# Performance work log

Hardware: AMD Instinct MI355X
Metric: run time of the kernel (lower is better)

The kernel has to match this reference:

```python
import jax, jax.numpy as jnp
import numpy as np

# MSDeformAttn dims inferred from Linear shapes: 8 heads * 4 levels * 2 points
H, L, P, D, C = 8, 4, 2, 32, 256
SHAPES = [(128, 128), (64, 64), (32, 32), (16, 16)]  # (H_l, W_l) per level
NV = sum(h * w for h, w in SHAPES)  # 21760
STARTS = np.cumsum([0] + [h * w for h, w in SHAPES])


def _bilinear(val, lx, ly, Hl, Wl):
    """grid_sample(align_corners=False, padding='zeros') equivalent.
    val: [B, H, Hl*Wl, D]; lx, ly: [B, H, N] normalized sample coords in [0,1].
    Returns [B, H, N, D]."""
    x = lx * Wl - 0.5
    y = ly * Hl - 0.5
    x0 = jnp.floor(x)
    y0 = jnp.floor(y)
    fx = x - x0
    fy = y - y0
    x0i = x0.astype(jnp.int32)
    y0i = y0.astype(jnp.int32)
    out = jnp.zeros(val.shape[:2] + (x.shape[-1], val.shape[-1]), val.dtype)
    corners = ((0, 0, (1 - fx) * (1 - fy)), (1, 0, fx * (1 - fy)),
               (0, 1, (1 - fx) * fy), (1, 1, fx * fy))
    for dx, dy, w in corners:
        xi = x0i + dx
        yi = y0i + dy
        valid = ((xi >= 0) & (xi < Wl) & (yi >= 0) & (yi < Hl)).astype(val.dtype)
        idx = jnp.clip(yi, 0, Hl - 1) * Wl + jnp.clip(xi, 0, Wl - 1)
        g = jnp.take_along_axis(val, idx[..., None], axis=2)  # [B,H,N,D]
        out = out + g * (w * valid)[..., None]
    return out


def setup_inputs() -> dict:
    key = jax.random.key(0)
    ks = jax.random.split(key, 8)
    B, NQ = 4, 1000
    s = 0.02
    return {
        "query": jax.random.normal(ks[0], (B, NQ, C), jnp.float32),
        "value": jax.random.normal(ks[1], (B, NV, C), jnp.float32),
        "reference_points": jax.random.uniform(ks[2], (B, NQ, L, 2), jnp.float32),
        "W_off": jax.random.normal(ks[3], (C, H * L * P * 2), jnp.float32) * s,
        "b_off": jnp.zeros((H * L * P * 2,), jnp.float32),
        "W_attn": jax.random.normal(ks[4], (C, H * L * P), jnp.float32) * s,
        "b_attn": jnp.zeros((H * L * P,), jnp.float32),
        "W_val": jax.random.normal(ks[5], (C, C), jnp.float32) * s,
        "b_val": jnp.zeros((C,), jnp.float32),
        "W_out": jax.random.normal(ks[6], (C, C), jnp.float32) * s,
        "b_out": jnp.zeros((C,), jnp.float32),
    }


def reference(query, value, reference_points, W_off, b_off, W_attn, b_attn,
              W_val, b_val, W_out, b_out):
    B, NQ, _ = query.shape
    # value projection -> per-head values [B, H, NV, D]
    v = (value @ W_val + b_val).reshape(B, NV, H, D).transpose(0, 2, 1, 3)
    # sampling offsets [B, NQ, H, L, P, 2]
    off = (query @ W_off + b_off).reshape(B, NQ, H, L, P, 2)
    # attention weights: softmax over L*P
    attn = jax.nn.softmax((query @ W_attn + b_attn).reshape(B, NQ, H, L * P), axis=-1)
    attn = attn.reshape(B, NQ, H, L, P)
    # normalizer (W_l, H_l) per level, matching Deformable-DETR
    wh = jnp.asarray([[w, h] for h, w in SHAPES], dtype=query.dtype)  # [L,2]
    loc = reference_points[:, :, None, :, None, :] + off / wh[None, None, None, :, None, :]
    out = jnp.zeros((B, H, NQ, D), dtype=query.dtype)
    for l, (hl, wl) in enumerate(SHAPES):
        vl = v[:, :, STARTS[l]:STARTS[l + 1], :]                 # [B,H,hl*wl,D]
        lx = loc[:, :, :, l, :, 0].transpose(0, 2, 1, 3).reshape(B, H, NQ * P)
        ly = loc[:, :, :, l, :, 1].transpose(0, 2, 1, 3).reshape(B, H, NQ * P)
        s = _bilinear(vl, lx, ly, hl, wl).reshape(B, H, NQ, P, D)
        al = attn[:, :, :, l, :].transpose(0, 2, 1, 3)           # [B,H,NQ,P]
        out = out + jnp.sum(s * al[..., None], axis=3)
    out = out.transpose(0, 2, 1, 3).reshape(B, NQ, C)
    return out @ W_out + b_out  # dropout(p=0) is identity
```

## Files before the change

### kernel.cpp

```cpp
#include <hip/hip_runtime.h>

#define HH 8
#define LL 4
#define PP 2
#define DD 32
#define CC 256
#define NVV 21760
#define NQQ 1000
#define BB 4
#define NQT (BB * NQQ)
#define NLOGB (NQT / 32)
#define NVALB ((BB * NVV) / 64)

typedef __attribute__((ext_vector_type(8))) short short8;
typedef __attribute__((ext_vector_type(4))) short shortv4;
typedef __attribute__((ext_vector_type(4))) float f32x4;

__device__ __forceinline__ unsigned short f2bf(float f) {
    unsigned u = __float_as_uint(f);
    u += 0x7FFF + ((u >> 16) & 1);
    return (unsigned short)(u >> 16);
}
__device__ __forceinline__ float bf2f(unsigned short h) {
    return __uint_as_float(((unsigned)h) << 16);
}
__device__ __forceinline__ unsigned cvtpk(float lo, float hi) {
    unsigned r;
    asm volatile("v_cvt_pk_bf16_f32 %0, %1, %2" : "=v"(r) : "v"(lo), "v"(hi));
    return r;
}

__device__ __forceinline__ void gload_lds16(const void* g, void* l) {
    __builtin_amdgcn_global_load_lds(
        (const __attribute__((address_space(1))) unsigned int*)g,
        (__attribute__((address_space(3))) unsigned int*)l, 16, 0, 0);
}

__global__ __launch_bounds__(256) void prep_kernel(
    const float* __restrict__ Wv, const float* __restrict__ Woff,
    const float* __restrict__ Wattn, const float* __restrict__ Wout,
    unsigned short* __restrict__ WTs, unsigned short* __restrict__ W1T,
    unsigned short* __restrict__ WoT)
{
    const int c = blockIdx.x;
    const int n = threadIdx.x;
    {
        int s = c >> 5, t = c & 31;
        WTs[s * 8192 + n * 32 + (t ^ (((n >> 1) & 3) << 3))] =
            f2bf(Wv[c * CC + n]);
    }
    if (n < 192) {
        float x = (n < 128) ? Woff[c * 128 + n] : Wattn[c * 64 + (n - 128)];
        W1T[n * CC + c] = f2bf(x);
    }
    WoT[n * CC + c] = f2bf(Wout[c * CC + n]);
}

__global__ __launch_bounds__(256, 3) void val_logits_fused(
    const float* __restrict__ value, const unsigned short* __restrict__ WTs,
    const float* __restrict__ bv, unsigned short* __restrict__ v_out,
    const float* __restrict__ query, const unsigned short* __restrict__ W1T,
    const float* __restrict__ b_off, const float* __restrict__ b_attn,
    float* __restrict__ logits)
{
    __shared__ __align__(16) char lds[49152];

    const int tid = threadIdx.x;
    const int lane = tid & 63;

    if (blockIdx.x >= NLOGB) {
        char (*Abuf)[8192] = (char (*)[8192])(lds);
        char (*Bbuf)[16384] = (char (*)[16384])(lds + 16384);

        const int w = tid >> 6;
        const int wm = w >> 1;
        const int wn = w & 1;
        const int lr = lane & 15;
        const int q = lane >> 4;
        const int bm = (blockIdx.x - NLOGB) * 64;

#define STAGE(s, bi)                                                        \
    {                                                                       \
        _Pragma("unroll") for (int r = 0; r < 2; ++r) {                     \
            int u = r * 256 + tid;                                          \
            int m = u >> 3, c = u & 7;                                      \
            gload_lds16((const char*)value + (size_t)(bm + m) * 1024 +      \
                            (s) * 128 + ((c ^ (m & 7)) * 16),               \
                        &Abuf[bi][u * 16]);                                 \
        }                                                                   \
        _Pragma("unroll") for (int r = 0; r < 4; ++r) {                     \
            int off = (r * 256 + tid) * 16;                                 \
            gload_lds16((const char*)WTs + (s) * 16384 + off,               \
                        &Bbuf[bi][off]);                                    \
        }                                                                   \
    }

        f32x4 acc[2][8] = {};

        STAGE(0, 0);
        STAGE(1, 1);

#pragma unroll
        for (int s = 0; s < 8; ++s) {
            const int cur = s & 1;
            if (s < 7) {
                asm volatile("s_waitcnt vmcnt(6)" ::: "memory");
            } else {
                asm volatile("s_waitcnt vmcnt(0)" ::: "memory");
            }
            __builtin_amdgcn_s_barrier();
            __builtin_amdgcn_sched_barrier(0);

            short8 af[2];
#pragma unroll
            for (int mf = 0; mf < 2; ++mf) {
                int m = wm * 32 + mf * 16 + lr;
                const char* base = &Abuf[cur][m * 128];
                f32x4 lo = *(const f32x4*)(base + (((2 * q) ^ (m & 7)) * 16));
                f32x4 hi =
                    *(const f32x4*)(base + (((2 * q + 1) ^ (m & 7)) * 16));
                uint4 uv = {cvtpk(lo[0], lo[1]), cvtpk(lo[2], lo[3]),
                            cvtpk(hi[0], hi[1]), cvtpk(hi[2], hi[3])};
                af[mf] = __builtin_bit_cast(short8, uv);
            }
#pragma unroll
            for (int nf = 0; nf < 8; ++nf) {
                int n = wn * 128 + nf * 16 + lr;
                short8 bf = *(const short8*)&Bbuf[cur]
                                [n * 64 + ((q ^ ((n >> 1) & 3)) * 16)];
                acc[0][nf] = __builtin_amdgcn_mfma_f32_16x16x32_bf16(
                    af[0], bf, acc[0][nf], 0, 0, 0);
                acc[1][nf] = __builtin_amdgcn_mfma_f32_16x16x32_bf16(
                    af[1], bf, acc[1][nf], 0, 0, 0);
            }

            __builtin_amdgcn_s_barrier();
            __builtin_amdgcn_sched_barrier(0);
            if (s < 6) STAGE(s + 2, cur);
        }
#undef STAGE

#pragma unroll
        for (int nf = 0; nf < 8; ++nf) {
            int col = wn * 128 + nf * 16 + lr;
            float bias = bv[col];
#pragma unroll
            for (int mf = 0; mf < 2; ++mf) {
                size_t rbase =
                    (size_t)(bm + wm * 32 + mf * 16 + q * 4) * 256 + col;
#pragma unroll
                for (int r = 0; r < 4; ++r)
                    v_out[rbase + (size_t)r * 256] =
                        f2bf(acc[mf][nf][r] + bias);
            }
        }
    } else {
        unsigned short (*As)[72] = (unsigned short (*)[72])(lds);
        unsigned short (*Bsl)[72] = (unsigned short (*)[72])(lds + 4608);

        const int wave = tid >> 6;
        const int bm = blockIdx.x * 32;
        const int lr = lane & 15;
        const int q = lane >> 4;
        f32x4 acc[2][3] = {};

        for (int k0 = 0; k0 < CC; k0 += 64) {
            float4 a[2];
            short8 wv[6];
#pragma unroll
            for (int i = 0; i < 2; ++i) {
                int u = tid + 256 * i;
                a[i] = *(const float4*)&query[(size_t)(bm + (u >> 4)) * CC +
                                              k0 + (u & 15) * 4];
            }
#pragma unroll
            for (int i = 0; i < 6; ++i) {
                int u = tid + 256 * i;
                wv[i] = *(const short8*)&W1T[(size_t)(u >> 3) * CC + k0 +
                                             (u & 7) * 8];
            }
            __syncthreads();
#pragma unroll
            for (int i = 0; i < 2; ++i) {
                int u = tid + 256 * i;
                shortv4 p;
                p[0] = (short)f2bf(a[i].x); p[1] = (short)f2bf(a[i].y);
                p[2] = (short)f2bf(a[i].z); p[3] = (short)f2bf(a[i].w);
                *(shortv4*)&As[u >> 4][(u & 15) * 4] = p;
            }
#pragma unroll
            for (int i = 0; i < 6; ++i) {
                int u = tid + 256 * i;
                *(short8*)&Bsl[u >> 3][(u & 7) * 8] = wv[i];
            }
            __syncthreads();

#pragma unroll
            for (int kk = 0; kk < 2; ++kk) {
                short8 afr[2], bfr[3];
#pragma unroll
                for (int mf = 0; mf < 2; ++mf)
                    afr[mf] = *(const short8*)&As[mf * 16 + lr][kk * 32 + q * 8];
#pragma unroll
                for (int nf = 0; nf < 3; ++nf)
                    bfr[nf] = *(const short8*)&Bsl[wave * 48 + nf * 16 + lr]
                                                 [kk * 32 + q * 8];
#pragma unroll
                for (int mf = 0; mf < 2; ++mf)
#pragma unroll
                    for (int nf = 0; nf < 3; ++nf)
                        acc[mf][nf] = __builtin_amdgcn_mfma_f32_16x16x32_bf16(
                            afr[mf], bfr[nf], acc[mf][nf], 0, 0, 0);
            }
            __syncthreads();
        }

#pragma unroll
        for (int nf = 0; nf < 3; ++nf) {
            int col = wave * 48 + nf * 16 + lr;
            float bias = (col < 128) ? b_off[col] : b_attn[col - 128];
#pragma unroll
            for (int mf = 0; mf < 2; ++mf)
#pragma unroll
                for (int r = 0; r < 4; ++r) {
                    int m = bm + mf * 16 + q * 4 + r;
                    logits[(size_t)m * 192 + col] = acc[mf][nf][r] + bias;
                }
        }
    }
}

__global__ __launch_bounds__(256) void sample_kernel(
    const float* __restrict__ logits,
    const float* __restrict__ refp,
    const unsigned short* __restrict__ v,
    unsigned short* __restrict__ mid)
{
    __shared__ float offl[128];
    __shared__ float attnl[64];
    __shared__ float refl[8];

    const int qy = blockIdx.x;
    const int b = qy / NQQ;
    const int tid = threadIdx.x;

    if (tid < 192) {
        float t = logits[(size_t)qy * 192 + tid];
        if (tid < 128) offl[tid] = t;
        else attnl[tid - 128] = t;
    } else if (tid < 200) {
        refl[tid - 192] = refp[(size_t)qy * 8 + (tid - 192)];
    }
    __syncthreads();

    if (tid < 8) {
        float m = -1e30f;
#pragma unroll
        for (int j = 0; j < 8; ++j) m = fmaxf(m, attnl[tid * 8 + j]);
        float s = 0.f, e[8];
#pragma unroll
        for (int j = 0; j < 8; ++j) {
            e[j] = __expf(attnl[tid * 8 + j] - m);
            s += e[j];
        }
        float inv = 1.f / s;
#pragma unroll
        for (int j = 0; j < 8; ++j) attnl[tid * 8 + j] = e[j] * inv;
    }
    __syncthreads();

    const int h = tid >> 5, d = tid & 31;
    const int starts[4] = {0, 16384, 20480, 21504};
    const float szs[4] = {128.f, 64.f, 32.f, 16.f};

    float acc = 0.f;
#pragma unroll
    for (int l = 0; l < LL; ++l) {
        const float S = szs[l];
        const int Wl = (int)S;
        const float refx = refl[l * 2 + 0];
        const float refy = refl[l * 2 + 1];
        const unsigned short* vl =
            v + (size_t)(b * NVV + starts[l]) * 256 + h * 32 + d;
#pragma unroll
        for (int p = 0; p < PP; ++p) {
            const int oi = h * 16 + l * 4 + p * 2;
            float lx = refx + offl[oi + 0] / S;
            float ly = refy + offl[oi + 1] / S;
            float x = lx * S - 0.5f;
            float y = ly * S - 0.5f;
            float x0f = floorf(x), y0f = floorf(y);
            float fx = x - x0f, fy = y - y0f;
            int x0 = (int)x0f, y0 = (int)y0f;
            float a = attnl[h * 8 + l * 2 + p];
            float sacc = 0.f;
#pragma unroll
            for (int dy = 0; dy < 2; ++dy) {
#pragma unroll
                for (int dx = 0; dx < 2; ++dx) {
                    int xi = x0 + dx, yi = y0 + dy;
                    float wgt = (dx ? fx : 1.f - fx) * (dy ? fy : 1.f - fy);
                    bool valid = (xi >= 0) && (xi < Wl) && (yi >= 0) && (yi < Wl);
                    int xc = min(max(xi, 0), Wl - 1);
                    int yc = min(max(yi, 0), Wl - 1);
                    float g = bf2f(vl[(size_t)(yc * Wl + xc) * 256]);
                    sacc += g * (valid ? wgt : 0.f);
                }
            }
            acc += a * sacc;
        }
    }
    mid[(size_t)qy * CC + h * 32 + d] = f2bf(acc);
}

__global__ __launch_bounds__(256) void out_mfma(
    const unsigned short* __restrict__ mid,
    const unsigned short* __restrict__ WoT, const float* __restrict__ b_out,
    float* __restrict__ out)
{
    __shared__ unsigned short As[32][72];
    __shared__ unsigned short Bso[256][72];
    const int tid = threadIdx.x;
    const int lane = tid & 63;
    const int wave = tid >> 6;
    const int bm = blockIdx.x * 32;
    const int lr = lane & 15;
    const int q = lane >> 4;
    f32x4 acc[2][4] = {};

    for (int k0 = 0; k0 < CC; k0 += 64) {
        short8 a0 = *(const short8*)&mid[(size_t)(bm + (tid >> 3)) * CC + k0 +
                                         (tid & 7) * 8];
        short8 wv[8];
#pragma unroll
        for (int i = 0; i < 8; ++i) {
            int u = tid + 256 * i;
            wv[i] = *(const short8*)&WoT[(size_t)(u >> 3) * CC + k0 + (u & 7) * 8];
        }
        __syncthreads();
        *(short8*)&As[tid >> 3][(tid & 7) * 8] = a0;
#pragma unroll
        for (int i = 0; i < 8; ++i) {
            int u = tid + 256 * i;
            *(short8*)&Bso[u >> 3][(u & 7) * 8] = wv[i];
        }
        __syncthreads();

#pragma unroll
        for (int kk = 0; kk < 2; ++kk) {
            short8 afr[2], bfr[4];
#pragma unroll
            for (int mf = 0; mf < 2; ++mf)
                afr[mf] = *(const short8*)&As[mf * 16 + lr][kk * 32 + q * 8];
#pragma unroll
            for (int nf = 0; nf < 4; ++nf)
                bfr[nf] =
                    *(const short8*)&Bso[wave * 64 + nf * 16 + lr][kk * 32 + q * 8];
#pragma unroll
            for (int mf = 0; mf < 2; ++mf)
#pragma unroll
                for (int nf = 0; nf < 4; ++nf)
                    acc[mf][nf] = __builtin_amdgcn_mfma_f32_16x16x32_bf16(
                        afr[mf], bfr[nf], acc[mf][nf], 0, 0, 0);
        }
        __syncthreads();
    }

#pragma unroll
    for (int nf = 0; nf < 4; ++nf) {
        int col = wave * 64 + nf * 16 + lr;
        float bias = b_out[col];
#pragma unroll
        for (int mf = 0; mf < 2; ++mf)
#pragma unroll
            for (int r = 0; r < 4; ++r) {
                int m = bm + mf * 16 + q * 4 + r;
                out[(size_t)m * CC + col] = acc[mf][nf][r] + bias;
            }
    }
}

extern "C" void kernel_launch(void* const* d_in, const int* in_sizes, int n_in,
                              void* d_out, int out_size, void* d_ws, size_t ws_size,
                              hipStream_t stream) {
    const float* query  = (const float*)d_in[0];
    const float* value  = (const float*)d_in[1];
    const float* refp   = (const float*)d_in[2];
    const float* W_off  = (const float*)d_in[3];
    const float* b_off  = (const float*)d_in[4];
    const float* W_attn = (const float*)d_in[5];
    const float* b_attn = (const float*)d_in[6];
    const float* W_val  = (const float*)d_in[7];
    const float* b_val  = (const float*)d_in[8];
    const float* W_out  = (const float*)d_in[9];
    const float* b_out  = (const float*)d_in[10];
    float* out = (float*)d_out;

    char* ws = (char*)d_ws;
    unsigned short* WTs    = (unsigned short*)(ws);
    unsigned short* v_ws   = (unsigned short*)(ws + 131072);
    unsigned short* W1T    = (unsigned short*)(ws + 44695552);
    unsigned short* WoT    = (unsigned short*)(ws + 44793856);
    float*          logits = (float*)(ws + 44924928);
    unsigned short* mid    = (unsigned short*)(ws + 47996928);

    prep_kernel<<<CC, 256, 0, stream>>>(W_val, W_off, W_attn, W_out,
                                        WTs, W1T, WoT);
    val_logits_fused<<<NLOGB + NVALB, 256, 0, stream>>>(
        value, WTs, b_val, v_ws, query, W1T, b_off, b_attn, logits);
    sample_kernel<<<NQT, 256, 0, stream>>>(logits, refp, v_ws, mid);
    out_mfma<<<NQT / 32, 256, 0, stream>>>(mid, WoT, b_out, out);
}
```

Baseline: 55.06 us.

## Fuse sampling with fp32 output projection, processing eight queries per block

Merges the bilinear sampling kernel and the MFMA output-projection GEMM into one kernel. Each block now handles 8 queries, keeps the sampled features in LDS, and applies W_out with scalar fp32 FMAs read straight from the fp32 input. This removes the intermediate mid buffer round-trip, one kernel launch, and the W_out bf16 conversion in prep. In exchange the projection runs on vector ALUs instead of matrix cores, and grid size drops to 500 blocks, which may hurt latency hiding in the gather phase.

```diff
diff --git a/kernel.cpp b/kernel.cpp
--- a/kernel.cpp
+++ b/kernel.cpp
@@ -11,6 +11,7 @@
 #define NQT (BB * NQQ)
 #define NLOGB (NQT / 32)
 #define NVALB ((BB * NVV) / 64)
+#define QB 8
 
 typedef __attribute__((ext_vector_type(8))) short short8;
 typedef __attribute__((ext_vector_type(4))) short shortv4;
@@ -38,9 +39,8 @@
 
 __global__ __launch_bounds__(256) void prep_kernel(
     const float* __restrict__ Wv, const float* __restrict__ Woff,
-    const float* __restrict__ Wattn, const float* __restrict__ Wout,
-    unsigned short* __restrict__ WTs, unsigned short* __restrict__ W1T,
-    unsigned short* __restrict__ WoT)
+    const float* __restrict__ Wattn,
+    unsigned short* __restrict__ WTs, unsigned short* __restrict__ W1T)
 {
     const int c = blockIdx.x;
     const int n = threadIdx.x;
@@ -53,7 +53,6 @@
         float x = (n < 128) ? Woff[c * 128 + n] : Wattn[c * 64 + (n - 128)];
         W1T[n * CC + c] = f2bf(x);
     }
-    WoT[n * CC + c] = f2bf(Wout[c * CC + n]);
 }
 
 __global__ __launch_bounds__(256, 3) void val_logits_fused(
@@ -230,42 +229,47 @@
     }
 }
 
-__global__ __launch_bounds__(256) void sample_kernel(
+__global__ __launch_bounds__(256) void sample_out_kernel(
     const float* __restrict__ logits,
     const float* __restrict__ refp,
     const unsigned short* __restrict__ v,
-    unsigned short* __restrict__ mid)
+    const float* __restrict__ W_out, const float* __restrict__ b_out,
+    float* __restrict__ out)
 {
-    __shared__ float offl[128];
-    __shared__ float attnl[64];
-    __shared__ float refl[8];
-
-    const int qy = blockIdx.x;
-    const int b = qy / NQQ;
+    __shared__ float offl[QB][128];
+    __shared__ float attnl[QB][64];
+    __shared__ float refl[QB][8];
+    __shared__ float midT[CC][QB];
+
+    const int bq0 = blockIdx.x * QB;
+    const int b = bq0 / NQQ;
     const int tid = threadIdx.x;
 
-    if (tid < 192) {
-        float t = logits[(size_t)qy * 192 + tid];
-        if (tid < 128) offl[tid] = t;
-        else attnl[tid - 128] = t;
-    } else if (tid < 200) {
-        refl[tid - 192] = refp[(size_t)qy * 8 + (tid - 192)];
-    }
+#pragma unroll
+    for (int qi = 0; qi < QB; ++qi) {
+        if (tid < 192) {
+            float t = logits[(size_t)(bq0 + qi) * 192 + tid];
+            if (tid < 128) offl[qi][tid] = t;
+            else attnl[qi][tid - 128] = t;
+        }
+    }
+    if (tid < QB * 8) refl[tid >> 3][tid & 7] = refp[(size_t)bq0 * 8 + tid];
     __syncthreads();
 
-    if (tid < 8) {
+    if (tid < QB * 8) {
+        int qi = tid >> 3, h = tid & 7;
         float m = -1e30f;
 #pragma unroll
-        for (int j = 0; j < 8; ++j) m = fmaxf(m, attnl[tid * 8 + j]);
+        for (int j = 0; j < 8; ++j) m = fmaxf(m, attnl[qi][h * 8 + j]);
         float s = 0.f, e[8];
 #pragma unroll
         for (int j = 0; j < 8; ++j) {
-            e[j] = __expf(attnl[tid * 8 + j] - m);
+            e[j] = __expf(attnl[qi][h * 8 + j] - m);
             s += e[j];
         }
         float inv = 1.f / s;
 #pragma unroll
-        for (int j = 0; j < 8; ++j) attnl[tid * 8 + j] = e[j] * inv;
+        for (int j = 0; j < 8; ++j) attnl[qi][h * 8 + j] = e[j] * inv;
     }
     __syncthreads();
 
@@ -273,110 +277,68 @@
     const int starts[4] = {0, 16384, 20480, 21504};
     const float szs[4] = {128.f, 64.f, 32.f, 16.f};
 
-    float acc = 0.f;
-#pragma unroll
-    for (int l = 0; l < LL; ++l) {
-        const float S = szs[l];
-        const int Wl = (int)S;
-        const float refx = refl[l * 2 + 0];
-        const float refy = refl[l * 2 + 1];
-        const unsigned short* vl =
-            v + (size_t)(b * NVV + starts[l]) * 256 + h * 32 + d;
-#pragma unroll
-        for (int p = 0; p < PP; ++p) {
-            const int oi = h * 16 + l * 4 + p * 2;
-            float lx = refx + offl[oi + 0] / S;
-            float ly = refy + offl[oi + 1] / S;
-            float x = lx * S - 0.5f;
-            float y = ly * S - 0.5f;
-            float x0f = floorf(x), y0f = floorf(y);
-            float fx = x - x0f, fy = y - y0f;
-            int x0 = (int)x0f, y0 = (int)y0f;
-            float a = attnl[h * 8 + l * 2 + p];
-            float sacc = 0.f;
-#pragma unroll
-            for (int dy = 0; dy < 2; ++dy) {
-#pragma unroll
-                for (int dx = 0; dx < 2; ++dx) {
-                    int xi = x0 + dx, yi = y0 + dy;
-                    float wgt = (dx ? fx : 1.f - fx) * (dy ? fy : 1.f - fy);
-                    bool valid = (xi >= 0) && (xi < Wl) && (yi >= 0) && (yi < Wl);
-                    int xc = min(max(xi, 0), Wl - 1);
-                    int yc = min(max(yi, 0), Wl - 1);
-                    float g = bf2f(vl[(size_t)(yc * Wl + xc) * 256]);
-                    sacc += g * (valid ? wgt : 0.f);
+#pragma unroll
+    for (int qi = 0; qi < QB; ++qi) {
+        float acc = 0.f;
+#pragma unroll
+        for (int l = 0; l < LL; ++l) {
+            const float S = szs[l];
+            const int Wl = (int)S;
+            const float refx = refl[qi][l * 2 + 0];
+            const float refy = refl[qi][l * 2 + 1];
+            const unsigned short* vl =
+                v + (size_t)(b * NVV + starts[l]) * 256 + h * 32 + d;
+#pragma unroll
+            for (int p = 0; p < PP; ++p) {
+                const int oi = h * 16 + l * 4 + p * 2;
+                float lx = refx + offl[qi][oi + 0] / S;
+                float ly = refy + offl[qi][oi + 1] / S;
+                float x = lx * S - 0.5f;
+                float y = ly * S - 0.5f;
+                float x0f = floorf(x), y0f = floorf(y);
+                float fx = x - x0f, fy = y - y0f;
+                int x0 = (int)x0f, y0 = (int)y0f;
+                float a = attnl[qi][h * 8 + l * 2 + p];
+                float sacc = 0.f;
+#pragma unroll
+                for (int dy = 0; dy < 2; ++dy) {
+#pragma unroll
+                    for (int dx = 0; dx < 2; ++dx) {
+                        int xi = x0 + dx, yi = y0 + dy;
+                        float wgt =
+                            (dx ? fx : 1.f - fx) * (dy ? fy : 1.f - fy);
+                        bool valid = (xi >= 0) && (xi < Wl) && (yi >= 0) &&
+                                     (yi < Wl);
+                        int xc = min(max(xi, 0), Wl - 1);
+                        int yc = min(max(yi, 0), Wl - 1);
+                        float g = bf2f(vl[(size_t)(yc * Wl + xc) * 256]);
+                        sacc += g * (valid ? wgt : 0.f);
+                    }
                 }
-            }
-            acc += a * sacc;
-        }
-    }
-    mid[(size_t)qy * CC + h * 32 + d] = f2bf(acc);
-}
-
-__global__ __launch_bounds__(256) void out_mfma(
-    const unsigned short* __restrict__ mid,
-    const unsigned short* __restrict__ WoT, const float* __restrict__ b_out,
-    float* __restrict__ out)
-{
-    __shared__ unsigned short As[32][72];
-    __shared__ unsigned short Bso[256][72];
-    const int tid = threadIdx.x;
-    const int lane = tid & 63;
-    const int wave = tid >> 6;
-    const int bm = blockIdx.x * 32;
-    const int lr = lane & 15;
-    const int q = lane >> 4;
-    f32x4 acc[2][4] = {};
-
-    for (int k0 = 0; k0 < CC; k0 += 64) {
-        short8 a0 = *(const short8*)&mid[(size_t)(bm + (tid >> 3)) * CC + k0 +
-                                         (tid & 7) * 8];
-        short8 wv[8];
-#pragma unroll
-        for (int i = 0; i < 8; ++i) {
-            int u = tid + 256 * i;
-            wv[i] = *(const short8*)&WoT[(size_t)(u >> 3) * CC + k0 + (u & 7) * 8];
-        }
-        __syncthreads();
-        *(short8*)&As[tid >> 3][(tid & 7) * 8] = a0;
-#pragma unroll
-        for (int i = 0; i < 8; ++i) {
-            int u = tid + 256 * i;
-            *(short8*)&Bso[u >> 3][(u & 7) * 8] = wv[i];
-        }
-        __syncthreads();
-
-#pragma unroll
-        for (int kk = 0; kk < 2; ++kk) {
-            short8 afr[2], bfr[4];
-#pragma unroll
-            for (int mf = 0; mf < 2; ++mf)
-                afr[mf] = *(const short8*)&As[mf * 16 + lr][kk * 32 + q * 8];
-#pragma unroll
-            for (int nf = 0; nf < 4; ++nf)
-                bfr[nf] =
-                    *(const short8*)&Bso[wave * 64 + nf * 16 + lr][kk * 32 + q * 8];
-#pragma unroll
-            for (int mf = 0; mf < 2; ++mf)
-#pragma unroll
-                for (int nf = 0; nf < 4; ++nf)
-                    acc[mf][nf] = __builtin_amdgcn_mfma_f32_16x16x32_bf16(
-                        afr[mf], bfr[nf], acc[mf][nf], 0, 0, 0);
-        }
-        __syncthreads();
-    }
-
-#pragma unroll
-    for (int nf = 0; nf < 4; ++nf) {
-        int col = wave * 64 + nf * 16 + lr;
-        float bias = b_out[col];
-#pragma unroll
-        for (int mf = 0; mf < 2; ++mf)
-#pragma unroll
-            for (int r = 0; r < 4; ++r) {
-                int m = bm + mf * 16 + q * 4 + r;
-                out[(size_t)m * CC + col] = acc[mf][nf][r] + bias;
-            }
+                acc += a * sacc;
+            }
+        }
+        midT[h * 32 + d][qi] = acc;
+    }
+    __syncthreads();
+
+    {
+        const int n = tid;
+        float accm[QB] = {};
+#pragma unroll 4
+        for (int c = 0; c < CC; ++c) {
+            float wv = W_out[(size_t)c * CC + n];
+            f32x4 m0 = *(const f32x4*)&midT[c][0];
+            f32x4 m1 = *(const f32x4*)&midT[c][4];
+            accm[0] += m0[0] * wv; accm[1] += m0[1] * wv;
+            accm[2] += m0[2] * wv; accm[3] += m0[3] * wv;
+            accm[4] += m1[0] * wv; accm[5] += m1[1] * wv;
+            accm[6] += m1[2] * wv; accm[7] += m1[3] * wv;
+        }
+        float bn = b_out[n];
+#pragma unroll
+        for (int qi = 0; qi < QB; ++qi)
+            out[(size_t)(bq0 + qi) * CC + n] = accm[qi] + bn;
     }
 }
 
@@ -400,14 +362,11 @@
     unsigned short* WTs    = (unsigned short*)(ws);
     unsigned short* v_ws   = (unsigned short*)(ws + 131072);
     unsigned short* W1T    = (unsigned short*)(ws + 44695552);
-    unsigned short* WoT    = (unsigned short*)(ws + 44793856);
-    float*          logits = (float*)(ws + 44924928);
-    unsigned short* mid    = (unsigned short*)(ws + 47996928);
-
-    prep_kernel<<<CC, 256, 0, stream>>>(W_val, W_off, W_attn, W_out,
-                                        WTs, W1T, WoT);
+    float*          logits = (float*)(ws + 44793856);
+
+    prep_kernel<<<CC, 256, 0, stream>>>(W_val, W_off, W_attn, WTs, W1T);
     val_logits_fused<<<NLOGB + NVALB, 256, 0, stream>>>(
         value, WTs, b_val, v_ws, query, W1T, b_off, b_attn, logits);
-    sample_kernel<<<NQT, 256, 0, stream>>>(logits, refp, v_ws, mid);
-    out_mfma<<<NQT / 32, 256, 0, stream>>>(mid, WoT, b_out, out);
-}
+    sample_out_kernel<<<NQT / QB, 256, 0, stream>>>(logits, refp, v_ws,
+                                                    W_out, b_out, out);
+}
```

New measurement: 71.15 us. +29.2%, slower.
